# Optimization experiments

Measured on AMD Instinct MI355X. Metric: run time of the kernel, lower is better.

The kernel has to match this reference:

```python
import jax, jax.numpy as jnp
import numpy as np

EPS = 1e-6
MAX_ITER = 3

def skew(w):
    z = jnp.zeros_like(w[:, 0])
    return jnp.stack([
        jnp.stack([z, -w[:, 2], w[:, 1]], -1),
        jnp.stack([w[:, 2], z, -w[:, 0]], -1),
        jnp.stack([-w[:, 1], w[:, 0], z], -1)], -2)

def twist2mat(w):
    # Rodrigues formula, w: [B,3] -> R: [B,3,3]
    theta = jnp.linalg.norm(w, axis=-1, keepdims=True) + 1e-12
    axis = w / theta
    Km = skew(axis)
    th = theta[..., None]
    I = jnp.eye(3, dtype=w.dtype)
    return I + jnp.sin(th) * Km + (1.0 - jnp.cos(th)) * (Km @ Km)

def sobel_gradient(img, normalize=True):
    # replicate-pad + 3x3 Sobel, img: [B,C,H,W]
    p = jnp.pad(img, ((0, 0), (0, 0), (1, 1), (1, 1)), mode='edge')
    tl = p[..., :-2, :-2]; tc = p[..., :-2, 1:-1]; tr = p[..., :-2, 2:]
    ml = p[..., 1:-1, :-2]; mr = p[..., 1:-1, 2:]
    bl = p[..., 2:, :-2]; bc = p[..., 2:, 1:-1]; br = p[..., 2:, 2:]
    dx = (tr - tl) + 2.0 * (mr - ml) + (br - bl)
    dy = (bl - tl) + 2.0 * (bc - tc) + (br - tr)
    if normalize:
        mag = jnp.sqrt(dx * dx + dy * dy + 1e-8)
        dx, dy = dx / mag, dy / mag
    return dx, dy

def _bilinear_one(F, u, v):
    # F: [C,H,W]; u,v: [H,W] pixel coords; border padding (grid_sample-like)
    C, H, W = F.shape
    u = jnp.clip(u, 0.0, W - 1.0)
    v = jnp.clip(v, 0.0, H - 1.0)
    x0 = jnp.floor(u); y0 = jnp.floor(v)
    wx = u - x0; wy = v - y0
    x0i = x0.astype(jnp.int32); y0i = y0.astype(jnp.int32)
    x1i = jnp.minimum(x0i + 1, W - 1); y1i = jnp.minimum(y0i + 1, H - 1)
    g = lambda yi, xi: F[:, yi, xi]  # advanced-index gather -> [C,H,W]
    return (g(y0i, x0i) * (1 - wx) * (1 - wy) + g(y0i, x1i) * wx * (1 - wy)
            + g(y1i, x0i) * (1 - wx) * wy + g(y1i, x1i) * wx * wy)

def warp_features(F, u, v):
    # F: [B,C,H,W]; u,v: [B,1,H,W]
    return jax.vmap(_bilinear_one)(F, u[:, 0], v[:, 0])

def generate_xy_grid(B, H, W, K):
    fx, fy, cx, cy = [K[:, i].reshape(B, 1, 1, 1) for i in range(4)]
    uu, vv = jnp.meshgrid(jnp.arange(W, dtype=K.dtype), jnp.arange(H, dtype=K.dtype))
    px = (uu[None, None] - cx) / fx
    py = (vv[None, None] - cy) / fy
    return px, py  # [B,1,H,W] each

def batch_warp_inverse_depth(px, py, invD0, R, t, K):
    B, _, H, W = px.shape
    xy1 = jnp.concatenate([px, py, jnp.ones_like(px)], 1).reshape(B, 3, -1)
    warped = R @ xy1 + t[:, :, None] * invD0.reshape(B, 1, -1)
    x_, y_, s_ = warped[:, 0], warped[:, 1], warped[:, 2]
    fx, fy, cx, cy = [K[:, i].reshape(B, 1) for i in range(4)]
    u_ = (x_ / s_ * fx + cx).reshape(B, 1, H, W)
    v_ = (y_ / s_ * fy + cy).reshape(B, 1, H, W)
    inv_z = invD0 / s_.reshape(B, 1, H, W)
    return u_, v_, inv_z

def check_occ(inv_z_buffer, invD1, u, v, thres=0.1):
    B, _, H, W = invD1.shape
    inv_z_warped = warp_features(invD1, u, v)
    inlier = inv_z_buffer > inv_z_warped - thres
    inview = (u > 0) & (u < W) & (v > 0) & (v < H)
    return ~(inlier & inview)  # [B,1,H,W] bool

def compute_jacobian_warping(invD, K, px, py):
    # linearized at origin (pose=None branch)
    B, _, H, W = invD.shape
    x = px.reshape(B, -1); y = py.reshape(B, -1); d = invD.reshape(B, -1)
    O = jnp.zeros_like(x)
    xy = x * y
    dx_dp = jnp.stack([-xy, 1.0 + x * x, -y, d, O, -d * x], -1)
    dy_dp = jnp.stack([-(1.0 + y * y), xy, x, O, d, -d * y], -1)
    fx = K[:, 0].reshape(B, 1, 1); fy = K[:, 1].reshape(B, 1, 1)
    return dx_dp * fx, dy_dp * fy  # [B,HW,6] each

def lev_mar_H(JtWJ):
    diag = jnp.eye(6, dtype=JtWJ.dtype)
    trace = jnp.trace(JtWJ, axis1=1, axis2=2)
    return JtWJ + (trace * 1e-6)[:, None, None] * diag

def forward(twist0, x0, x1, invD0, invD1, sigma0, sigma1, K):
    B, C, H, W = x0.shape
    N = H * W
    dtype = x0.dtype
    R = twist2mat(twist0[:, :3])
    t = twist0[:, 3:]
    px, py = generate_xy_grid(B, H, W, K)
    # inverse-compositional: template Jacobian precomputed once
    Jf_x, Jf_y = sobel_gradient(x0, normalize=True)
    Jx_p, Jy_p = compute_jacobian_warping(invD0, K, px, py)
    J = (Jf_x.reshape(B, C, N, 1) * Jx_p.reshape(B, 1, N, 6)
         + Jf_y.reshape(B, C, N, 1) * Jy_p.reshape(B, 1, N, 6))  # [B,C,N,6]
    for _ in range(MAX_ITER):
        u_w, v_w, inv_z = batch_warp_inverse_depth(px, py, invD0, R, t, K)
        occ = check_occ(inv_z, invD1, u_w, v_w)
        f_r = warp_features(x1, u_w, v_w)
        sigma_r = warp_features(sigma1, u_w, v_w)
        res = f_r - x0
        sigma = jnp.sqrt(sigma_r * sigma_r + sigma0 * sigma0)
        wres = jnp.where(occ, EPS, res / sigma)  # [B,C,H,W]
        valid = (~occ).reshape(B, 1, N, 1).astype(dtype)
        Jw = (J / sigma.reshape(B, C, N, 1) * valid).reshape(B, C * N, 6)
        r = jnp.where(occ, 0.0, wres).reshape(B, C * N)
        JtWJ = jnp.einsum('bnk,bnl->bkl', Jw, Jw)
        Rhs = jnp.einsum('bnk,bn->bk', Jw, r)[..., None]
        xi = jnp.linalg.solve(lev_mar_H(JtWJ), Rhs)  # [B,6,1]
        d_R = twist2mat(-xi[:, :3, 0])
        d_t = -(d_R @ xi[:, 3:])
        t = (R @ d_t)[:, :, 0] + t
        R = R @ d_R
    return jnp.concatenate([R.reshape(B, 9), t], axis=1)  # [B,12]

def setup_inputs() -> dict:
    key = jax.random.key(0)
    ks = jax.random.split(key, 7)
    B, C, H, W = 8, 16, 240, 320
    twist0 = jax.random.normal(ks[0], (B, 6), jnp.float32) * 0.01
    x0 = jax.random.normal(ks[1], (B, C, H, W), jnp.float32)
    x1 = jax.random.normal(ks[2], (B, C, H, W), jnp.float32)
    invD0 = jax.random.uniform(ks[3], (B, 1, H, W), jnp.float32, 0.1, 1.0)
    invD1 = jax.random.uniform(ks[4], (B, 1, H, W), jnp.float32, 0.1, 1.0)
    sigma0 = jax.random.uniform(ks[5], (B, C, H, W), jnp.float32, 0.1, 1.0)
    sigma1 = jax.random.uniform(ks[6], (B, C, H, W), jnp.float32, 0.1, 1.0)
    Kmat = jnp.tile(jnp.array([[0.8 * W, 0.8 * W, W / 2.0, H / 2.0]], jnp.float32), (B, 1))
    return dict(twist0=twist0, x0=x0, x1=x1, invD0=invD0, invD1=invD1,
                sigma0=sigma0, sigma1=sigma1, K=Kmat)

def reference(twist0, x0, x1, invD0, invD1, sigma0, sigma1, K):
    return forward(twist0, x0, x1, invD0, invD1, sigma0, sigma1, K)
```

## Files before the change

### kernel.cpp

```cpp
#include <hip/hip_runtime.h>
#include <hip/hip_fp16.h>

#define B_ 8
#define C_ 16
#define H_ 240
#define W_ 320
#define N_ (H_*W_)

__device__ __forceinline__ void twist2mat_dev(float w0, float w1, float w2, float R[9]) {
    float th = sqrtf(w0*w0 + w1*w1 + w2*w2) + 1e-12f;
    float ax = w0/th, ay = w1/th, az = w2/th;
    float s = sinf(th), c = cosf(th), ic = 1.0f - c;
    R[0] = 1.0f + ic*(ax*ax - 1.0f);
    R[1] = -s*az + ic*ax*ay;
    R[2] =  s*ay + ic*ax*az;
    R[3] =  s*az + ic*ax*ay;
    R[4] = 1.0f + ic*(ay*ay - 1.0f);
    R[5] = -s*ax + ic*ay*az;
    R[6] = -s*ay + ic*ax*az;
    R[7] =  s*ax + ic*ay*az;
    R[8] = 1.0f + ic*(az*az - 1.0f);
}

__device__ __forceinline__ unsigned pack_h2(float a, float b) {
    __half2 h = __floats2half2_rn(a, b);
    return *reinterpret_cast<unsigned*>(&h);
}
__device__ __forceinline__ float2 unpack_h2(unsigned u) {
    __half2 h = *reinterpret_cast<__half2*>(&u);
    return __half22float2(h);
}

__device__ __forceinline__ void solve_update(const float* __restrict__ ac, float R[9], float t[3]) {
    float M[6][7];
    {
        int idx = 0;
        #pragma unroll
        for (int k = 0; k < 6; k++)
            #pragma unroll
            for (int l = k; l < 6; l++) { M[k][l] = ac[idx]; M[l][k] = ac[idx]; idx++; }
    }
    const float trace = M[0][0]+M[1][1]+M[2][2]+M[3][3]+M[4][4]+M[5][5];
    const float lam = trace * 1e-6f;
    #pragma unroll
    for (int i = 0; i < 6; i++) { M[i][i] += lam; M[i][6] = ac[21+i]; }

    #pragma unroll
    for (int k = 0; k < 6; k++) {
        const float inv = 1.0f / M[k][k];
        #pragma unroll
        for (int i = k+1; i < 6; i++) {
            const float f = M[i][k] * inv;
            #pragma unroll
            for (int j = k; j < 7; j++) M[i][j] -= f * M[k][j];
        }
    }
    float xi[6];
    #pragma unroll
    for (int i = 5; i >= 0; i--) {
        float s = M[i][6];
        #pragma unroll
        for (int j = i+1; j < 6; j++) s -= M[i][j]*xi[j];
        xi[i] = s / M[i][i];
    }

    float dR[9];
    twist2mat_dev(-xi[0], -xi[1], -xi[2], dR);
    const float dt0 = -(dR[0]*xi[3] + dR[1]*xi[4] + dR[2]*xi[5]);
    const float dt1 = -(dR[3]*xi[3] + dR[4]*xi[4] + dR[5]*xi[5]);
    const float dt2 = -(dR[6]*xi[3] + dR[7]*xi[4] + dR[8]*xi[5]);

    const float nt0 = R[0]*dt0 + R[1]*dt1 + R[2]*dt2 + t[0];
    const float nt1 = R[3]*dt0 + R[4]*dt1 + R[5]*dt2 + t[1];
    const float nt2 = R[6]*dt0 + R[7]*dt1 + R[8]*dt2 + t[2];
    float nR[9];
    #pragma unroll
    for (int i = 0; i < 3; i++)
        #pragma unroll
        for (int j = 0; j < 3; j++)
            nR[i*3+j] = R[i*3+0]*dR[0*3+j] + R[i*3+1]*dR[1*3+j] + R[i*3+2]*dR[2*3+j];
    #pragma unroll
    for (int i = 0; i < 9; i++) R[i] = nR[i];
    t[0] = nt0; t[1] = nt1; t[2] = nt2;
}

__device__ __forceinline__ void build_RT(const float* __restrict__ twist0,
                                         const float* __restrict__ accum,
                                         int b, int iters, float R[9], float t[3]) {
    const float* w = twist0 + b*6;
    twist2mat_dev(w[0], w[1], w[2], R);
    t[0] = w[3]; t[1] = w[4]; t[2] = w[5];
    for (int j = 0; j < iters; j++)
        solve_update(accum + (size_t)(j*B_ + b)*27, R, t);
}

__launch_bounds__(256)
__global__ void precompute_kernel(const float* __restrict__ x0, const float* __restrict__ x1,
                                  const float* __restrict__ sigma0, const float* __restrict__ sigma1,
                                  uint4* __restrict__ P0h, uint4* __restrict__ X1S1h,
                                  float* __restrict__ accum)
{
    if (blockIdx.x == 0 && blockIdx.y == 0 && blockIdx.z == 0) {
        for (int k = threadIdx.x; k < 3*B_*27; k += 256) accum[k] = 0.0f;
    }
    const int pix = blockIdx.x*256 + threadIdx.x;
    const int cg = blockIdx.y;
    const int b = blockIdx.z;
    const int h = pix / W_, w = pix - h*W_;
    const int hm = max(h-1,0), hp = min(h+1,H_-1);
    const int wm = max(w-1,0), wp = min(w+1,W_-1);

    unsigned p0[8];
    unsigned xsp[4];
    #pragma unroll
    for (int i = 0; i < 4; i++) {
        const int c = cg*4 + i;
        const size_t base = ((size_t)(b*C_+c))*N_;
        const float* xc = x0 + base;
        const float tl = xc[hm*W_+wm], tc_ = xc[hm*W_+w], tr = xc[hm*W_+wp];
        const float ml = xc[h*W_+wm],                     mr = xc[h*W_+wp];
        const float bl = xc[hp*W_+wm], bc_ = xc[hp*W_+w], br = xc[hp*W_+wp];
        const float dx = tr - tl + 2.0f*(mr - ml) + (br - bl);
        const float dy = bl - tl + 2.0f*(bc_ - tc_) + (br - tr);
        const float mag = sqrtf(dx*dx + dy*dy + 1e-8f);
        const float s0v = sigma0[base + pix];
        p0[i*2+0] = pack_h2(dx/mag, dy/mag);
        p0[i*2+1] = pack_h2(xc[pix], s0v*s0v);
        xsp[i] = pack_h2(x1[base + pix], sigma1[base + pix]);
    }
    uint4 a; a.x = p0[0]; a.y = p0[1]; a.z = p0[2]; a.w = p0[3];
    uint4 bb; bb.x = p0[4]; bb.y = p0[5]; bb.z = p0[6]; bb.w = p0[7];
    P0h[((size_t)(b*8 + cg*2  ))*N_ + pix] = a;
    P0h[((size_t)(b*8 + cg*2+1))*N_ + pix] = bb;
    uint4 q; q.x = xsp[0]; q.y = xsp[1]; q.z = xsp[2]; q.w = xsp[3];
    X1S1h[((size_t)(b*4 + cg))*N_ + pix] = q;
}

__launch_bounds__(256)
__global__ void iter_kernel(const uint4* __restrict__ P0h, const uint4* __restrict__ X1S1h,
                            const float* __restrict__ invD0, const float* __restrict__ invD1,
                            const float* __restrict__ Kmat, const float* __restrict__ twist0,
                            float* __restrict__ accum, int it)
{
    const int b = blockIdx.y;
    const int pix = blockIdx.x * 256 + threadIdx.x;
    const int h = pix / W_;
    const int w = pix - h*W_;

    float Rm[9], tv[3];
    build_RT(twist0, accum, b, it, Rm, tv);

    const float fx = Kmat[b*4+0], fy = Kmat[b*4+1], cx = Kmat[b*4+2], cy = Kmat[b*4+3];

    float acc[27];
    #pragma unroll
    for (int j = 0; j < 27; j++) acc[j] = 0.0f;

    const float px = ((float)w - cx) / fx;
    const float py = ((float)h - cy) / fy;
    const float d  = invD0[b*N_ + pix];

    const float x_ = Rm[0]*px + Rm[1]*py + Rm[2] + tv[0]*d;
    const float y_ = Rm[3]*px + Rm[4]*py + Rm[5] + tv[1]*d;
    const float s_ = Rm[6]*px + Rm[7]*py + Rm[8] + tv[2]*d;
    const float u = x_/s_*fx + cx;
    const float v = y_/s_*fy + cy;
    const float inv_z = d / s_;

    const float uc = fminf(fmaxf(u, 0.0f), (float)(W_-1));
    const float vc = fminf(fmaxf(v, 0.0f), (float)(H_-1));
    const float x0f = floorf(uc), y0f = floorf(vc);
    const float wx = uc - x0f, wy = vc - y0f;
    const int x0i = (int)x0f, y0i = (int)y0f;
    const int x1i = min(x0i+1, W_-1), y1i = min(y0i+1, H_-1);
    const float w00 = (1.0f-wx)*(1.0f-wy), w01 = wx*(1.0f-wy);
    const float w10 = (1.0f-wx)*wy,        w11 = wx*wy;
    const int i00 = y0i*W_+x0i, i01 = y0i*W_+x1i, i10 = y1i*W_+x0i, i11 = y1i*W_+x1i;

    const float* dz = invD1 + b*N_;
    const float zw = dz[i00]*w00 + dz[i01]*w01 + dz[i10]*w10 + dz[i11]*w11;
    const bool inlier = inv_z > zw - 0.1f;
    const bool inview = (u > 0.0f) && (u < (float)W_) && (v > 0.0f) && (v < (float)H_);
    const bool valid  = inlier && inview;

    if (valid) {
        const float xy = px*py;
        const float Av[6] = { -xy*fx, (1.0f+px*px)*fx, -py*fx, d*fx, 0.0f, -d*px*fx };
        const float Bv[6] = { -(1.0f+py*py)*fy, xy*fy, px*fy, 0.0f, d*fy, -d*py*fy };

        float Swxx=0.f, Swxy=0.f, Swyy=0.f, Srx=0.f, Sry=0.f;
        const uint4* P0b   = P0h   + (size_t)b*8*N_;
        const uint4* X1S1b = X1S1h + (size_t)b*4*N_;

#define CH(gword, xword, t00, t01, t10, t11) { \
        const float2 g  = unpack_h2(gword); \
        const float2 xs = unpack_h2(xword); \
        const float2 a00 = unpack_h2(t00), a01 = unpack_h2(t01), \
                     a10 = unpack_h2(t10), a11 = unpack_h2(t11); \
        const float fr = a00.x*w00 + a01.x*w01 + a10.x*w10 + a11.x*w11; \
        const float sr = a00.y*w00 + a01.y*w01 + a10.y*w10 + a11.y*w11; \
        const float inv_s2 = 1.0f/(sr*sr + xs.y); \
        const float res = fr - xs.x; \
        const float gxw = g.x*inv_s2, gyw = g.y*inv_s2; \
        Swxx += g.x*gxw; Swxy += g.x*gyw; Swyy += g.y*gyw; \
        Srx  += res*gxw; Sry  += res*gyw; }

        #pragma unroll
        for (int cg = 0; cg < 4; cg++) {
            const uint4 pA = P0b[(size_t)(cg*2  )*N_ + pix];
            const uint4 pB = P0b[(size_t)(cg*2+1)*N_ + pix];
            const uint4* xsb = X1S1b + (size_t)cg*N_;
            const uint4 q00 = xsb[i00], q01 = xsb[i01], q10 = xsb[i10], q11 = xsb[i11];
            CH(pA.x, pA.y, q00.x, q01.x, q10.x, q11.x)
            CH(pA.z, pA.w, q00.y, q01.y, q10.y, q11.y)
            CH(pB.x, pB.y, q00.z, q01.z, q10.z, q11.z)
            CH(pB.z, pB.w, q00.w, q01.w, q10.w, q11.w)
        }
#undef CH

        int idx = 0;
        #pragma unroll
        for (int k = 0; k < 6; k++) {
            #pragma unroll
            for (int l = k; l < 6; l++) {
                acc[idx++] = Swxx*Av[k]*Av[l] + Swxy*(Av[k]*Bv[l] + Bv[k]*Av[l]) + Swyy*Bv[k]*Bv[l];
            }
        }
        #pragma unroll
        for (int k = 0; k < 6; k++) acc[21+k] = Srx*Av[k] + Sry*Bv[k];
    }

    const int lane = threadIdx.x & 63;
    const int wave = threadIdx.x >> 6;
    __shared__ float red[4][27];
    #pragma unroll
    for (int j = 0; j < 27; j++) {
        float vv = acc[j];
        vv += __shfl_down(vv, 32);
        vv += __shfl_down(vv, 16);
        vv += __shfl_down(vv, 8);
        vv += __shfl_down(vv, 4);
        vv += __shfl_down(vv, 2);
        vv += __shfl_down(vv, 1);
        if (lane == 0) red[wave][j] = vv;
    }
    __syncthreads();
    if (threadIdx.x < 27) {
        float s = red[0][threadIdx.x] + red[1][threadIdx.x] + red[2][threadIdx.x] + red[3][threadIdx.x];
        atomicAdd(&accum[(size_t)(it*B_ + b)*27 + threadIdx.x], s);
    }
}

__global__ void finalize_kernel(const float* __restrict__ twist0, const float* __restrict__ accum,
                                float* __restrict__ out)
{
    const int b = threadIdx.x;
    if (b >= B_) return;
    float Rm[9], tv[3];
    build_RT(twist0, accum, b, 3, Rm, tv);
    float* ob = out + b*12;
    #pragma unroll
    for (int i = 0; i < 9; i++) ob[i] = Rm[i];
    ob[9] = tv[0]; ob[10] = tv[1]; ob[11] = tv[2];
}

extern "C" void kernel_launch(void* const* d_in, const int* in_sizes, int n_in,
                              void* d_out, int out_size, void* d_ws, size_t ws_size,
                              hipStream_t stream) {
    const float* twist0 = (const float*)d_in[0];
    const float* x0     = (const float*)d_in[1];
    const float* x1     = (const float*)d_in[2];
    const float* invD0  = (const float*)d_in[3];
    const float* invD1  = (const float*)d_in[4];
    const float* sigma0 = (const float*)d_in[5];
    const float* sigma1 = (const float*)d_in[6];
    const float* Kmat   = (const float*)d_in[7];
    float* out = (float*)d_out;

    const size_t p0_bytes = (size_t)B_*8*N_*sizeof(uint4);
    const size_t xs_bytes = (size_t)B_*4*N_*sizeof(uint4);

    uint4* P0h   = (uint4*)d_ws;
    uint4* X1S1h = (uint4*)((char*)d_ws + p0_bytes);
    float* accum = (float*)((char*)d_ws + p0_bytes + xs_bytes);

    hipLaunchKernelGGL(precompute_kernel, dim3(N_/256, 4, B_), dim3(256), 0, stream,
                       x0, x1, sigma0, sigma1, P0h, X1S1h, accum);

    dim3 grid(N_/256, B_);
    for (int it = 0; it < 3; ++it) {
        hipLaunchKernelGGL(iter_kernel, grid, dim3(256), 0, stream,
                           P0h, X1S1h, invD0, invD1, Kmat, twist0, accum, it);
    }
    hipLaunchKernelGGL(finalize_kernel, dim3(1), dim3(64), 0, stream, twist0, accum, out);
}
```

Measured before the change: 362.1 us.

## Fuse Gauss-Newton iterations into a persistent cooperative kernel with grid sync

Replaces the three per-iteration launches and the finalize launch with one cooperative persistent kernel. Blocks loop over pixel tiles, and a grid-wide sync separates the iterations. Block 0 writes the final pose at the end. This removes launch gaps between the iterations and the finalize step, at the cost of lower parallelism per iteration (grid capped at occupancy) and the cost of the grid barrier. The cg loop unroll also drops from full to 2, which may reduce register pressure.

Result: slower. 727.5 us (+100.9%).

```diff
diff --git a/kernel.cpp b/kernel.cpp
--- a/kernel.cpp
+++ b/kernel.cpp
@@ -1,11 +1,16 @@
 #include <hip/hip_runtime.h>
 #include <hip/hip_fp16.h>
+#include <hip/hip_cooperative_groups.h>
+
+namespace cgns = cooperative_groups;
 
 #define B_ 8
 #define C_ 16
 #define H_ 240
 #define W_ 320
 #define N_ (H_*W_)
+#define TPB 300
+#define NTILES (B_*TPB)
 
 __device__ __forceinline__ void twist2mat_dev(float w0, float w1, float w2, float R[9]) {
     float th = sqrtf(w0*w0 + w1*w1 + w2*w2) + 1e-12f;
@@ -31,7 +36,7 @@
     return __half22float2(h);
 }
 
-__device__ __forceinline__ void solve_update(const float* __restrict__ ac, float R[9], float t[3]) {
+__device__ __forceinline__ void solve_update(const float* ac, float R[9], float t[3]) {
     float M[6][7];
     {
         int idx = 0;
@@ -84,8 +89,7 @@
     t[0] = nt0; t[1] = nt1; t[2] = nt2;
 }
 
-__device__ __forceinline__ void build_RT(const float* __restrict__ twist0,
-                                         const float* __restrict__ accum,
+__device__ __forceinline__ void build_RT(const float* twist0, const float* accum,
                                          int b, int iters, float R[9], float t[3]) {
     const float* w = twist0 + b*6;
     twist2mat_dev(w[0], w[1], w[2], R);
@@ -136,29 +140,19 @@
     X1S1h[((size_t)(b*4 + cg))*N_ + pix] = q;
 }
 
-__launch_bounds__(256)
-__global__ void iter_kernel(const uint4* __restrict__ P0h, const uint4* __restrict__ X1S1h,
-                            const float* __restrict__ invD0, const float* __restrict__ invD1,
-                            const float* __restrict__ Kmat, const float* __restrict__ twist0,
-                            float* __restrict__ accum, int it)
-{
-    const int b = blockIdx.y;
-    const int pix = blockIdx.x * 256 + threadIdx.x;
+__device__ __forceinline__ void accum_pixel(const uint4* __restrict__ P0b,
+                                            const uint4* __restrict__ X1S1b,
+                                            const float* __restrict__ invD0b,
+                                            const float* __restrict__ invD1b,
+                                            float fx, float fy, float cx, float cy,
+                                            const float Rm[9], const float tv[3],
+                                            int pix, float acc[27])
+{
     const int h = pix / W_;
     const int w = pix - h*W_;
-
-    float Rm[9], tv[3];
-    build_RT(twist0, accum, b, it, Rm, tv);
-
-    const float fx = Kmat[b*4+0], fy = Kmat[b*4+1], cx = Kmat[b*4+2], cy = Kmat[b*4+3];
-
-    float acc[27];
-    #pragma unroll
-    for (int j = 0; j < 27; j++) acc[j] = 0.0f;
-
     const float px = ((float)w - cx) / fx;
     const float py = ((float)h - cy) / fy;
-    const float d  = invD0[b*N_ + pix];
+    const float d  = invD0b[pix];
 
     const float x_ = Rm[0]*px + Rm[1]*py + Rm[2] + tv[0]*d;
     const float y_ = Rm[3]*px + Rm[4]*py + Rm[5] + tv[1]*d;
@@ -177,62 +171,60 @@
     const float w10 = (1.0f-wx)*wy,        w11 = wx*wy;
     const int i00 = y0i*W_+x0i, i01 = y0i*W_+x1i, i10 = y1i*W_+x0i, i11 = y1i*W_+x1i;
 
-    const float* dz = invD1 + b*N_;
-    const float zw = dz[i00]*w00 + dz[i01]*w01 + dz[i10]*w10 + dz[i11]*w11;
+    const float zw = invD1b[i00]*w00 + invD1b[i01]*w01 + invD1b[i10]*w10 + invD1b[i11]*w11;
     const bool inlier = inv_z > zw - 0.1f;
     const bool inview = (u > 0.0f) && (u < (float)W_) && (v > 0.0f) && (v < (float)H_);
-    const bool valid  = inlier && inview;
-
-    if (valid) {
-        const float xy = px*py;
-        const float Av[6] = { -xy*fx, (1.0f+px*px)*fx, -py*fx, d*fx, 0.0f, -d*px*fx };
-        const float Bv[6] = { -(1.0f+py*py)*fy, xy*fy, px*fy, 0.0f, d*fy, -d*py*fy };
-
-        float Swxx=0.f, Swxy=0.f, Swyy=0.f, Srx=0.f, Sry=0.f;
-        const uint4* P0b   = P0h   + (size_t)b*8*N_;
-        const uint4* X1S1b = X1S1h + (size_t)b*4*N_;
+    if (!(inlier && inview)) return;
+
+    const float xy = px*py;
+    const float Av[6] = { -xy*fx, (1.0f+px*px)*fx, -py*fx, d*fx, 0.0f, -d*px*fx };
+    const float Bv[6] = { -(1.0f+py*py)*fy, xy*fy, px*fy, 0.0f, d*fy, -d*py*fy };
+
+    float Swxx=0.f, Swxy=0.f, Swyy=0.f, Srx=0.f, Sry=0.f;
 
 #define CH(gword, xword, t00, t01, t10, t11) { \
-        const float2 g  = unpack_h2(gword); \
-        const float2 xs = unpack_h2(xword); \
-        const float2 a00 = unpack_h2(t00), a01 = unpack_h2(t01), \
-                     a10 = unpack_h2(t10), a11 = unpack_h2(t11); \
-        const float fr = a00.x*w00 + a01.x*w01 + a10.x*w10 + a11.x*w11; \
-        const float sr = a00.y*w00 + a01.y*w01 + a10.y*w10 + a11.y*w11; \
-        const float inv_s2 = 1.0f/(sr*sr + xs.y); \
-        const float res = fr - xs.x; \
-        const float gxw = g.x*inv_s2, gyw = g.y*inv_s2; \
-        Swxx += g.x*gxw; Swxy += g.x*gyw; Swyy += g.y*gyw; \
-        Srx  += res*gxw; Sry  += res*gyw; }
-
-        #pragma unroll
-        for (int cg = 0; cg < 4; cg++) {
-            const uint4 pA = P0b[(size_t)(cg*2  )*N_ + pix];
-            const uint4 pB = P0b[(size_t)(cg*2+1)*N_ + pix];
-            const uint4* xsb = X1S1b + (size_t)cg*N_;
-            const uint4 q00 = xsb[i00], q01 = xsb[i01], q10 = xsb[i10], q11 = xsb[i11];
-            CH(pA.x, pA.y, q00.x, q01.x, q10.x, q11.x)
-            CH(pA.z, pA.w, q00.y, q01.y, q10.y, q11.y)
-            CH(pB.x, pB.y, q00.z, q01.z, q10.z, q11.z)
-            CH(pB.z, pB.w, q00.w, q01.w, q10.w, q11.w)
+    const float2 g  = unpack_h2(gword); \
+    const float2 xs = unpack_h2(xword); \
+    const float2 a00 = unpack_h2(t00), a01 = unpack_h2(t01), \
+                 a10 = unpack_h2(t10), a11 = unpack_h2(t11); \
+    const float fr = a00.x*w00 + a01.x*w01 + a10.x*w10 + a11.x*w11; \
+    const float sr = a00.y*w00 + a01.y*w01 + a10.y*w10 + a11.y*w11; \
+    const float inv_s2 = 1.0f/(sr*sr + xs.y); \
+    const float res = fr - xs.x; \
+    const float gxw = g.x*inv_s2, gyw = g.y*inv_s2; \
+    Swxx += g.x*gxw; Swxy += g.x*gyw; Swyy += g.y*gyw; \
+    Srx  += res*gxw; Sry  += res*gyw; }
+
+    #pragma unroll 2
+    for (int cg = 0; cg < 4; cg++) {
+        const uint4 pA = P0b[(size_t)(cg*2  )*N_ + pix];
+        const uint4 pB = P0b[(size_t)(cg*2+1)*N_ + pix];
+        const uint4* xsb = X1S1b + (size_t)cg*N_;
+        const uint4 q00 = xsb[i00], q01 = xsb[i01], q10 = xsb[i10], q11 = xsb[i11];
+        CH(pA.x, pA.y, q00.x, q01.x, q10.x, q11.x)
+        CH(pA.z, pA.w, q00.y, q01.y, q10.y, q11.y)
+        CH(pB.x, pB.y, q00.z, q01.z, q10.z, q11.z)
+        CH(pB.z, pB.w, q00.w, q01.w, q10.w, q11.w)
+    }
+#undef CH
+
+    int idx = 0;
+    #pragma unroll
+    for (int k = 0; k < 6; k++) {
+        #pragma unroll
+        for (int l = k; l < 6; l++) {
+            acc[idx++] += Swxx*Av[k]*Av[l] + Swxy*(Av[k]*Bv[l] + Bv[k]*Av[l]) + Swyy*Bv[k]*Bv[l];
         }
-#undef CH
-
-        int idx = 0;
-        #pragma unroll
-        for (int k = 0; k < 6; k++) {
-            #pragma unroll
-            for (int l = k; l < 6; l++) {
-                acc[idx++] = Swxx*Av[k]*Av[l] + Swxy*(Av[k]*Bv[l] + Bv[k]*Av[l]) + Swyy*Bv[k]*Bv[l];
-            }
-        }
-        #pragma unroll
-        for (int k = 0; k < 6; k++) acc[21+k] = Srx*Av[k] + Sry*Bv[k];
-    }
-
-    const int lane = threadIdx.x & 63;
-    const int wave = threadIdx.x >> 6;
-    __shared__ float red[4][27];
+    }
+    #pragma unroll
+    for (int k = 0; k < 6; k++) acc[21+k] += Srx*Av[k] + Sry*Bv[k];
+}
+
+__device__ __forceinline__ void block_reduce_atomic(float acc[27], float* dst,
+                                                    float red[4][27], int tid)
+{
+    const int lane = tid & 63;
+    const int wave = tid >> 6;
     #pragma unroll
     for (int j = 0; j < 27; j++) {
         float vv = acc[j];
@@ -245,10 +237,81 @@
         if (lane == 0) red[wave][j] = vv;
     }
     __syncthreads();
-    if (threadIdx.x < 27) {
-        float s = red[0][threadIdx.x] + red[1][threadIdx.x] + red[2][threadIdx.x] + red[3][threadIdx.x];
-        atomicAdd(&accum[(size_t)(it*B_ + b)*27 + threadIdx.x], s);
-    }
+    if (tid < 27) {
+        float s = red[0][tid] + red[1][tid] + red[2][tid] + red[3][tid];
+        atomicAdd(&dst[tid], s);
+    }
+    __syncthreads();
+}
+
+__launch_bounds__(256)
+__global__ void solve_iters_coop(const uint4* __restrict__ P0h, const uint4* __restrict__ X1S1h,
+                                 const float* __restrict__ invD0, const float* __restrict__ invD1,
+                                 const float* __restrict__ Kmat, const float* __restrict__ twist0,
+                                 float* __restrict__ accum, float* __restrict__ out)
+{
+    cgns::grid_group grid = cgns::this_grid();
+    const int tid = threadIdx.x;
+    __shared__ float red[4][27];
+
+    for (int it = 0; it < 3; ++it) {
+        for (int tile = blockIdx.x; tile < NTILES; tile += gridDim.x) {
+            const int b  = tile / TPB;
+            const int pt = tile - b*TPB;
+            const int pix = pt*256 + tid;
+
+            float Rm[9], tv[3];
+            build_RT(twist0, accum, b, it, Rm, tv);
+
+            const float fx = Kmat[b*4+0], fy = Kmat[b*4+1], cx = Kmat[b*4+2], cy = Kmat[b*4+3];
+            float acc[27];
+            #pragma unroll
+            for (int j = 0; j < 27; j++) acc[j] = 0.0f;
+
+            accum_pixel(P0h + (size_t)b*8*N_, X1S1h + (size_t)b*4*N_,
+                        invD0 + (size_t)b*N_, invD1 + (size_t)b*N_,
+                        fx, fy, cx, cy, Rm, tv, pix, acc);
+
+            block_reduce_atomic(acc, &accum[(size_t)(it*B_ + b)*27], red, tid);
+        }
+        __threadfence();
+        grid.sync();
+    }
+
+    if (blockIdx.x == 0 && tid < B_) {
+        float Rm[9], tv[3];
+        build_RT(twist0, accum, tid, 3, Rm, tv);
+        float* ob = out + tid*12;
+        #pragma unroll
+        for (int i = 0; i < 9; i++) ob[i] = Rm[i];
+        ob[9] = tv[0]; ob[10] = tv[1]; ob[11] = tv[2];
+    }
+}
+
+__launch_bounds__(256)
+__global__ void iter_kernel_fb(const uint4* __restrict__ P0h, const uint4* __restrict__ X1S1h,
+                               const float* __restrict__ invD0, const float* __restrict__ invD1,
+                               const float* __restrict__ Kmat, const float* __restrict__ twist0,
+                               float* __restrict__ accum, int it)
+{
+    const int b = blockIdx.y;
+    const int pix = blockIdx.x*256 + threadIdx.x;
+    const int tid = threadIdx.x;
+    __shared__ float red[4][27];
+
+    float Rm[9], tv[3];
+    build_RT(twist0, accum, b, it, Rm, tv);
+
+    const float fx = Kmat[b*4+0], fy = Kmat[b*4+1], cx = Kmat[b*4+2], cy = Kmat[b*4+3];
+    float acc[27];
+    #pragma unroll
+    for (int j = 0; j < 27; j++) acc[j] = 0.0f;
+
+    accum_pixel(P0h + (size_t)b*8*N_, X1S1h + (size_t)b*4*N_,
+                invD0 + (size_t)b*N_, invD1 + (size_t)b*N_,
+                fx, fy, cx, cy, Rm, tv, pix, acc);
+
+    block_reduce_atomic(acc, &accum[(size_t)(it*B_ + b)*27], red, tid);
 }
 
 __global__ void finalize_kernel(const float* __restrict__ twist0, const float* __restrict__ accum,
@@ -287,10 +350,28 @@
     hipLaunchKernelGGL(precompute_kernel, dim3(N_/256, 4, B_), dim3(256), 0, stream,
                        x0, x1, sigma0, sigma1, P0h, X1S1h, accum);
 
-    dim3 grid(N_/256, B_);
-    for (int it = 0; it < 3; ++it) {
-        hipLaunchKernelGGL(iter_kernel, grid, dim3(256), 0, stream,
-                           P0h, X1S1h, invD0, invD1, Kmat, twist0, accum, it);
-    }
-    hipLaunchKernelGGL(finalize_kernel, dim3(1), dim3(64), 0, stream, twist0, accum, out);
-}
+    int blocksPerCU = 0;
+    (void)hipOccupancyMaxActiveBlocksPerMultiprocessor(&blocksPerCU, solve_iters_coop, 256, 0);
+    int numCU = 0;
+    (void)hipDeviceGetAttribute(&numCU, hipDeviceAttributeMultiprocessorCount, 0);
+
+    bool coop_ok = false;
+    if (blocksPerCU > 0 && numCU > 0) {
+        int nblk = blocksPerCU * numCU;
+        if (nblk > NTILES) nblk = NTILES;
+        void* args[] = { (void*)&P0h, (void*)&X1S1h, (void*)&invD0, (void*)&invD1,
+                         (void*)&Kmat, (void*)&twist0, (void*)&accum, (void*)&out };
+        hipError_t e = hipLaunchCooperativeKernel((const void*)solve_iters_coop,
+                                                  dim3(nblk), dim3(256), args, 0, stream);
+        coop_ok = (e == hipSuccess);
+    }
+
+    if (!coop_ok) {
+        dim3 grid(TPB, B_);
+        for (int it = 0; it < 3; ++it) {
+            hipLaunchKernelGGL(iter_kernel_fb, grid, dim3(256), 0, stream,
+                               P0h, X1S1h, invD0, invD1, Kmat, twist0, accum, it);
+        }
+        hipLaunchKernelGGL(finalize_kernel, dim3(1), dim3(64), 0, stream, twist0, accum, out);
+    }
+}
```

## Fuse precompute with first iteration and solve pose in last-block epilogue

Applied to the files above, without the earlier changes.

Merges the precompute kernel with iteration 0. Each block computes its share of the iteration-0 normal equations from the fp32 values it just loaded, and reads full-precision bilinear samples of x1 and sigma1 for its four channels. A last-block ticket epilogue then solves the 6x6 system and writes R,t into a buffer, which removes the finalize kernel and the per-thread replay of earlier solves in every block. This adds a memset, atomics and fences, plus a `#pragma unroll 2` in the channel loop. The fused iteration 0 now does extra scattered fp32 gathers from global memory.

After: 720.8 us. 1.99x slower.

```diff
diff --git a/kernel.cpp b/kernel.cpp
--- a/kernel.cpp
+++ b/kernel.cpp
@@ -6,6 +6,8 @@
 #define H_ 240
 #define W_ 320
 #define N_ (H_*W_)
+#define K1_BLOCKS_PER_B (300*4)
+#define K2_BLOCKS_PER_B 300
 
 __device__ __forceinline__ void twist2mat_dev(float w0, float w1, float w2, float R[9]) {
     float th = sqrtf(w0*w0 + w1*w1 + w2*w2) + 1e-12f;
@@ -31,19 +33,19 @@
     return __half22float2(h);
 }
 
-__device__ __forceinline__ void solve_update(const float* __restrict__ ac, float R[9], float t[3]) {
+__device__ __forceinline__ void solve_update(const float* sums, float R[9], float t[3]) {
     float M[6][7];
     {
         int idx = 0;
         #pragma unroll
         for (int k = 0; k < 6; k++)
             #pragma unroll
-            for (int l = k; l < 6; l++) { M[k][l] = ac[idx]; M[l][k] = ac[idx]; idx++; }
+            for (int l = k; l < 6; l++) { M[k][l] = sums[idx]; M[l][k] = sums[idx]; idx++; }
     }
     const float trace = M[0][0]+M[1][1]+M[2][2]+M[3][3]+M[4][4]+M[5][5];
     const float lam = trace * 1e-6f;
     #pragma unroll
-    for (int i = 0; i < 6; i++) { M[i][i] += lam; M[i][6] = ac[21+i]; }
+    for (int i = 0; i < 6; i++) { M[i][i] += lam; M[i][6] = sums[21+i]; }
 
     #pragma unroll
     for (int k = 0; k < 6; k++) {
@@ -84,34 +86,83 @@
     t[0] = nt0; t[1] = nt1; t[2] = nt2;
 }
 
-__device__ __forceinline__ void build_RT(const float* __restrict__ twist0,
-                                         const float* __restrict__ accum,
-                                         int b, int iters, float R[9], float t[3]) {
-    const float* w = twist0 + b*6;
-    twist2mat_dev(w[0], w[1], w[2], R);
-    t[0] = w[3]; t[1] = w[4]; t[2] = w[5];
-    for (int j = 0; j < iters; j++)
-        solve_update(accum + (size_t)(j*B_ + b)*27, R, t);
+__device__ __forceinline__ void block_reduce_atomic(float acc[27], float* dst,
+                                                    float red[4][27], int tid)
+{
+    const int lane = tid & 63;
+    const int wave = tid >> 6;
+    #pragma unroll
+    for (int j = 0; j < 27; j++) {
+        float vv = acc[j];
+        vv += __shfl_down(vv, 32);
+        vv += __shfl_down(vv, 16);
+        vv += __shfl_down(vv, 8);
+        vv += __shfl_down(vv, 4);
+        vv += __shfl_down(vv, 2);
+        vv += __shfl_down(vv, 1);
+        if (lane == 0) red[wave][j] = vv;
+    }
+    __syncthreads();
+    if (tid < 27) {
+        float s = red[0][tid] + red[1][tid] + red[2][tid] + red[3][tid];
+        atomicAdd(&dst[tid], s);
+    }
+}
+
+__device__ __forceinline__ void epilogue_solve(int it, int b,
+                                               const float* __restrict__ twist0,
+                                               float* __restrict__ accum,
+                                               float* __restrict__ RTbuf,
+                                               float* __restrict__ out, int lane)
+{
+    __threadfence();
+    float* ac = accum + (size_t)(it*B_ + b)*27;
+    float sv = 0.0f;
+    if (lane < 27) sv = atomicAdd(&ac[lane], 0.0f);
+    float sums[27];
+    #pragma unroll
+    for (int j = 0; j < 27; j++) sums[j] = __shfl(sv, j);
+
+    float R[9], t[3];
+    if (it == 0) {
+        const float* w = twist0 + b*6;
+        twist2mat_dev(w[0], w[1], w[2], R);
+        t[0] = w[3]; t[1] = w[4]; t[2] = w[5];
+    } else {
+        const float* rt = RTbuf + (size_t)(it*B_ + b)*12;
+        #pragma unroll
+        for (int i = 0; i < 9; i++) R[i] = rt[i];
+        t[0] = rt[9]; t[1] = rt[10]; t[2] = rt[11];
+    }
+    solve_update(sums, R, t);
+
+    if (lane == 0) {
+        float* dst = (it == 2) ? (out + b*12) : (RTbuf + (size_t)((it+1)*B_ + b)*12);
+        #pragma unroll
+        for (int i = 0; i < 9; i++) dst[i] = R[i];
+        dst[9] = t[0]; dst[10] = t[1]; dst[11] = t[2];
+    }
 }
 
 __launch_bounds__(256)
-__global__ void precompute_kernel(const float* __restrict__ x0, const float* __restrict__ x1,
-                                  const float* __restrict__ sigma0, const float* __restrict__ sigma1,
-                                  uint4* __restrict__ P0h, uint4* __restrict__ X1S1h,
-                                  float* __restrict__ accum)
+__global__ void fused_pre_iter0(const float* __restrict__ x0, const float* __restrict__ x1,
+                                const float* __restrict__ sigma0, const float* __restrict__ sigma1,
+                                const float* __restrict__ invD0, const float* __restrict__ invD1,
+                                const float* __restrict__ Kmat, const float* __restrict__ twist0,
+                                uint4* __restrict__ P0h, uint4* __restrict__ X1S1h,
+                                float* __restrict__ accum, float* __restrict__ RTbuf,
+                                unsigned* __restrict__ tickets, float* __restrict__ out)
 {
-    if (blockIdx.x == 0 && blockIdx.y == 0 && blockIdx.z == 0) {
-        for (int k = threadIdx.x; k < 3*B_*27; k += 256) accum[k] = 0.0f;
-    }
     const int pix = blockIdx.x*256 + threadIdx.x;
     const int cg = blockIdx.y;
     const int b = blockIdx.z;
+    const int tid = threadIdx.x;
     const int h = pix / W_, w = pix - h*W_;
     const int hm = max(h-1,0), hp = min(h+1,H_-1);
     const int wm = max(w-1,0), wp = min(w+1,W_-1);
 
-    unsigned p0[8];
-    unsigned xsp[4];
+    float gx[4], gy[4], x0c[4], s0sq[4];
+    unsigned p0[8], xsp[4];
     #pragma unroll
     for (int i = 0; i < 4; i++) {
         const int c = cg*4 + i;
@@ -123,42 +174,33 @@
         const float dx = tr - tl + 2.0f*(mr - ml) + (br - bl);
         const float dy = bl - tl + 2.0f*(bc_ - tc_) + (br - tr);
         const float mag = sqrtf(dx*dx + dy*dy + 1e-8f);
+        gx[i] = dx/mag; gy[i] = dy/mag;
+        x0c[i] = xc[pix];
         const float s0v = sigma0[base + pix];
-        p0[i*2+0] = pack_h2(dx/mag, dy/mag);
-        p0[i*2+1] = pack_h2(xc[pix], s0v*s0v);
+        s0sq[i] = s0v*s0v;
+        p0[i*2+0] = pack_h2(gx[i], gy[i]);
+        p0[i*2+1] = pack_h2(x0c[i], s0sq[i]);
         xsp[i] = pack_h2(x1[base + pix], sigma1[base + pix]);
     }
-    uint4 a; a.x = p0[0]; a.y = p0[1]; a.z = p0[2]; a.w = p0[3];
-    uint4 bb; bb.x = p0[4]; bb.y = p0[5]; bb.z = p0[6]; bb.w = p0[7];
-    P0h[((size_t)(b*8 + cg*2  ))*N_ + pix] = a;
-    P0h[((size_t)(b*8 + cg*2+1))*N_ + pix] = bb;
-    uint4 q; q.x = xsp[0]; q.y = xsp[1]; q.z = xsp[2]; q.w = xsp[3];
-    X1S1h[((size_t)(b*4 + cg))*N_ + pix] = q;
-}
-
-__launch_bounds__(256)
-__global__ void iter_kernel(const uint4* __restrict__ P0h, const uint4* __restrict__ X1S1h,
-                            const float* __restrict__ invD0, const float* __restrict__ invD1,
-                            const float* __restrict__ Kmat, const float* __restrict__ twist0,
-                            float* __restrict__ accum, int it)
-{
-    const int b = blockIdx.y;
-    const int pix = blockIdx.x * 256 + threadIdx.x;
-    const int h = pix / W_;
-    const int w = pix - h*W_;
+    {
+        uint4 a; a.x = p0[0]; a.y = p0[1]; a.z = p0[2]; a.w = p0[3];
+        uint4 bb; bb.x = p0[4]; bb.y = p0[5]; bb.z = p0[6]; bb.w = p0[7];
+        P0h[((size_t)(b*8 + cg*2  ))*N_ + pix] = a;
+        P0h[((size_t)(b*8 + cg*2+1))*N_ + pix] = bb;
+        uint4 q; q.x = xsp[0]; q.y = xsp[1]; q.z = xsp[2]; q.w = xsp[3];
+        X1S1h[((size_t)(b*4 + cg))*N_ + pix] = q;
+    }
 
     float Rm[9], tv[3];
-    build_RT(twist0, accum, b, it, Rm, tv);
-
+    {
+        const float* wv = twist0 + b*6;
+        twist2mat_dev(wv[0], wv[1], wv[2], Rm);
+        tv[0] = wv[3]; tv[1] = wv[4]; tv[2] = wv[5];
+    }
     const float fx = Kmat[b*4+0], fy = Kmat[b*4+1], cx = Kmat[b*4+2], cy = Kmat[b*4+3];
-
-    float acc[27];
-    #pragma unroll
-    for (int j = 0; j < 27; j++) acc[j] = 0.0f;
-
     const float px = ((float)w - cx) / fx;
     const float py = ((float)h - cy) / fy;
-    const float d  = invD0[b*N_ + pix];
+    const float d  = invD0[(size_t)b*N_ + pix];
 
     const float x_ = Rm[0]*px + Rm[1]*py + Rm[2] + tv[0]*d;
     const float y_ = Rm[3]*px + Rm[4]*py + Rm[5] + tv[1]*d;
@@ -177,13 +219,115 @@
     const float w10 = (1.0f-wx)*wy,        w11 = wx*wy;
     const int i00 = y0i*W_+x0i, i01 = y0i*W_+x1i, i10 = y1i*W_+x0i, i11 = y1i*W_+x1i;
 
-    const float* dz = invD1 + b*N_;
+    const float* dz = invD1 + (size_t)b*N_;
     const float zw = dz[i00]*w00 + dz[i01]*w01 + dz[i10]*w10 + dz[i11]*w11;
     const bool inlier = inv_z > zw - 0.1f;
     const bool inview = (u > 0.0f) && (u < (float)W_) && (v > 0.0f) && (v < (float)H_);
-    const bool valid  = inlier && inview;
-
-    if (valid) {
+
+    float acc[27];
+    #pragma unroll
+    for (int j = 0; j < 27; j++) acc[j] = 0.0f;
+
+    if (inlier && inview) {
+        const float xy = px*py;
+        const float Av[6] = { -xy*fx, (1.0f+px*px)*fx, -py*fx, d*fx, 0.0f, -d*px*fx };
+        const float Bv[6] = { -(1.0f+py*py)*fy, xy*fy, px*fy, 0.0f, d*fy, -d*py*fy };
+
+        float Swxx=0.f, Swxy=0.f, Swyy=0.f, Srx=0.f, Sry=0.f;
+        #pragma unroll
+        for (int i = 0; i < 4; i++) {
+            const int c = cg*4 + i;
+            const size_t base = ((size_t)(b*C_+c))*N_;
+            const float* x1c = x1 + base;
+            const float* s1c = sigma1 + base;
+            const float fr = x1c[i00]*w00 + x1c[i01]*w01 + x1c[i10]*w10 + x1c[i11]*w11;
+            const float sr = s1c[i00]*w00 + s1c[i01]*w01 + s1c[i10]*w10 + s1c[i11]*w11;
+            const float inv_s2 = 1.0f / (sr*sr + s0sq[i]);
+            const float res = fr - x0c[i];
+            const float gxw = gx[i]*inv_s2, gyw = gy[i]*inv_s2;
+            Swxx += gx[i]*gxw;
+            Swxy += gx[i]*gyw;
+            Swyy += gy[i]*gyw;
+            Srx  += res*gxw;
+            Sry  += res*gyw;
+        }
+        int idx = 0;
+        #pragma unroll
+        for (int k = 0; k < 6; k++) {
+            #pragma unroll
+            for (int l = k; l < 6; l++) {
+                acc[idx++] = Swxx*Av[k]*Av[l] + Swxy*(Av[k]*Bv[l] + Bv[k]*Av[l]) + Swyy*Bv[k]*Bv[l];
+            }
+        }
+        #pragma unroll
+        for (int k = 0; k < 6; k++) acc[21+k] = Srx*Av[k] + Sry*Bv[k];
+    }
+
+    __shared__ float red[4][27];
+    block_reduce_atomic(acc, &accum[(size_t)(0*B_ + b)*27], red, tid);
+
+    __shared__ unsigned lastFlag;
+    if (tid == 0) {
+        __threadfence();
+        unsigned prev = atomicAdd(&tickets[0*B_ + b], 1u);
+        lastFlag = (prev == K1_BLOCKS_PER_B - 1) ? 1u : 0u;
+    }
+    __syncthreads();
+    if (lastFlag && tid < 64) {
+        epilogue_solve(0, b, twist0, accum, RTbuf, out, tid);
+    }
+}
+
+__launch_bounds__(256)
+__global__ void iter_mid(const uint4* __restrict__ P0h, const uint4* __restrict__ X1S1h,
+                         const float* __restrict__ invD0, const float* __restrict__ invD1,
+                         const float* __restrict__ Kmat, const float* __restrict__ twist0,
+                         float* __restrict__ accum, float* __restrict__ RTbuf,
+                         unsigned* __restrict__ tickets, float* __restrict__ out, int it)
+{
+    const int b = blockIdx.y;
+    const int pix = blockIdx.x*256 + threadIdx.x;
+    const int tid = threadIdx.x;
+    const int h = pix / W_;
+    const int w = pix - h*W_;
+
+    const float* rt = RTbuf + (size_t)(it*B_ + b)*12;
+    const float R00=rt[0],R01=rt[1],R02=rt[2],R10=rt[3],R11=rt[4],R12=rt[5],
+                R20=rt[6],R21=rt[7],R22=rt[8];
+    const float t0=rt[9], t1=rt[10], t2=rt[11];
+    const float fx = Kmat[b*4+0], fy = Kmat[b*4+1], cx = Kmat[b*4+2], cy = Kmat[b*4+3];
+
+    const float px = ((float)w - cx) / fx;
+    const float py = ((float)h - cy) / fy;
+    const float d  = invD0[(size_t)b*N_ + pix];
+
+    const float x_ = R00*px + R01*py + R02 + t0*d;
+    const float y_ = R10*px + R11*py + R12 + t1*d;
+    const float s_ = R20*px + R21*py + R22 + t2*d;
+    const float u = x_/s_*fx + cx;
+    const float v = y_/s_*fy + cy;
+    const float inv_z = d / s_;
+
+    const float uc = fminf(fmaxf(u, 0.0f), (float)(W_-1));
+    const float vc = fminf(fmaxf(v, 0.0f), (float)(H_-1));
+    const float x0f = floorf(uc), y0f = floorf(vc);
+    const float wx = uc - x0f, wy = vc - y0f;
+    const int x0i = (int)x0f, y0i = (int)y0f;
+    const int x1i = min(x0i+1, W_-1), y1i = min(y0i+1, H_-1);
+    const float w00 = (1.0f-wx)*(1.0f-wy), w01 = wx*(1.0f-wy);
+    const float w10 = (1.0f-wx)*wy,        w11 = wx*wy;
+    const int i00 = y0i*W_+x0i, i01 = y0i*W_+x1i, i10 = y1i*W_+x0i, i11 = y1i*W_+x1i;
+
+    const float* dz = invD1 + (size_t)b*N_;
+    const float zw = dz[i00]*w00 + dz[i01]*w01 + dz[i10]*w10 + dz[i11]*w11;
+    const bool inlier = inv_z > zw - 0.1f;
+    const bool inview = (u > 0.0f) && (u < (float)W_) && (v > 0.0f) && (v < (float)H_);
+
+    float acc[27];
+    #pragma unroll
+    for (int j = 0; j < 27; j++) acc[j] = 0.0f;
+
+    if (inlier && inview) {
         const float xy = px*py;
         const float Av[6] = { -xy*fx, (1.0f+px*px)*fx, -py*fx, d*fx, 0.0f, -d*px*fx };
         const float Bv[6] = { -(1.0f+py*py)*fy, xy*fy, px*fy, 0.0f, d*fy, -d*py*fy };
@@ -205,11 +349,11 @@
         Swxx += g.x*gxw; Swxy += g.x*gyw; Swyy += g.y*gyw; \
         Srx  += res*gxw; Sry  += res*gyw; }
 
-        #pragma unroll
-        for (int cg = 0; cg < 4; cg++) {
-            const uint4 pA = P0b[(size_t)(cg*2  )*N_ + pix];
-            const uint4 pB = P0b[(size_t)(cg*2+1)*N_ + pix];
-            const uint4* xsb = X1S1b + (size_t)cg*N_;
+        #pragma unroll 2
+        for (int cgi = 0; cgi < 4; cgi++) {
+            const uint4 pA = P0b[(size_t)(cgi*2  )*N_ + pix];
+            const uint4 pB = P0b[(size_t)(cgi*2+1)*N_ + pix];
+            const uint4* xsb = X1S1b + (size_t)cgi*N_;
             const uint4 q00 = xsb[i00], q01 = xsb[i01], q10 = xsb[i10], q11 = xsb[i11];
             CH(pA.x, pA.y, q00.x, q01.x, q10.x, q11.x)
             CH(pA.z, pA.w, q00.y, q01.y, q10.y, q11.y)
@@ -230,38 +374,19 @@
         for (int k = 0; k < 6; k++) acc[21+k] = Srx*Av[k] + Sry*Bv[k];
     }
 
-    const int lane = threadIdx.x & 63;
-    const int wave = threadIdx.x >> 6;
     __shared__ float red[4][27];
-    #pragma unroll
-    for (int j = 0; j < 27; j++) {
-        float vv = acc[j];
-        vv += __shfl_down(vv, 32);
-        vv += __shfl_down(vv, 16);
-        vv += __shfl_down(vv, 8);
-        vv += __shfl_down(vv, 4);
-        vv += __shfl_down(vv, 2);
-        vv += __shfl_down(vv, 1);
-        if (lane == 0) red[wave][j] = vv;
+    block_reduce_atomic(acc, &accum[(size_t)(it*B_ + b)*27], red, tid);
+
+    __shared__ unsigned lastFlag;
+    if (tid == 0) {
+        __threadfence();
+        unsigned prev = atomicAdd(&tickets[it*B_ + b], 1u);
+        lastFlag = (prev == K2_BLOCKS_PER_B - 1) ? 1u : 0u;
     }
     __syncthreads();
-    if (threadIdx.x < 27) {
-        float s = red[0][threadIdx.x] + red[1][threadIdx.x] + red[2][threadIdx.x] + red[3][threadIdx.x];
-        atomicAdd(&accum[(size_t)(it*B_ + b)*27 + threadIdx.x], s);
-    }
-}
-
-__global__ void finalize_kernel(const float* __restrict__ twist0, const float* __restrict__ accum,
-                                float* __restrict__ out)
-{
-    const int b = threadIdx.x;
-    if (b >= B_) return;
-    float Rm[9], tv[3];
-    build_RT(twist0, accum, b, 3, Rm, tv);
-    float* ob = out + b*12;
-    #pragma unroll
-    for (int i = 0; i < 9; i++) ob[i] = Rm[i];
-    ob[9] = tv[0]; ob[10] = tv[1]; ob[11] = tv[2];
+    if (lastFlag && tid < 64) {
+        epilogue_solve(it, b, twist0, accum, RTbuf, out, tid);
+    }
 }
 
 extern "C" void kernel_launch(void* const* d_in, const int* in_sizes, int n_in,
@@ -282,15 +407,23 @@
 
     uint4* P0h   = (uint4*)d_ws;
     uint4* X1S1h = (uint4*)((char*)d_ws + p0_bytes);
-    float* accum = (float*)((char*)d_ws + p0_bytes + xs_bytes);
-
-    hipLaunchKernelGGL(precompute_kernel, dim3(N_/256, 4, B_), dim3(256), 0, stream,
-                       x0, x1, sigma0, sigma1, P0h, X1S1h, accum);
+    char*  smal  = (char*)d_ws + p0_bytes + xs_bytes;
+    float*    accum   = (float*)smal;
+    float*    RTbuf   = accum + 3*B_*27;
+    unsigned* tickets = (unsigned*)(RTbuf + 3*B_*12);
+    const size_t small_bytes = (3*B_*27 + 3*B_*12)*sizeof(float) + 3*B_*sizeof(unsigned);
+
+    hipMemsetAsync(smal, 0, small_bytes, stream);
+
+    hipLaunchKernelGGL(fused_pre_iter0, dim3(N_/256, 4, B_), dim3(256), 0, stream,
+                       x0, x1, sigma0, sigma1, invD0, invD1, Kmat, twist0,
+                       P0h, X1S1h, accum, RTbuf, tickets, out);
 
     dim3 grid(N_/256, B_);
-    for (int it = 0; it < 3; ++it) {
-        hipLaunchKernelGGL(iter_kernel, grid, dim3(256), 0, stream,
-                           P0h, X1S1h, invD0, invD1, Kmat, twist0, accum, it);
-    }
-    hipLaunchKernelGGL(finalize_kernel, dim3(1), dim3(64), 0, stream, twist0, accum, out);
-}
+    hipLaunchKernelGGL(iter_mid, grid, dim3(256), 0, stream,
+                       P0h, X1S1h, invD0, invD1, Kmat, twist0,
+                       accum, RTbuf, tickets, out, 1);
+    hipLaunchKernelGGL(iter_mid, grid, dim3(256), 0, stream,
+                       P0h, X1S1h, invD0, invD1, Kmat, twist0,
+                       accum, RTbuf, tickets, out, 2);
+}
```
